# Kernel optimization log

Measured on AMD Instinct MI355X. Metric: run time of the kernel, lower is better.

The kernel has to match this reference:

```python
import jax, jax.numpy as jnp
import numpy as np

B_, S, D_IN, D_OUT, N_ADP, R = 4, 4096, 2048, 2048, 4, 16
SCALE = 32.0 / 16.0  # lora_alpha / r, use_rslora=False, same for all adaptors


def setup_inputs() -> dict:
    key = jax.random.key(0)
    ks = jax.random.split(key, 6)
    x = jax.random.normal(ks[0], (B_, S, D_IN), dtype=jnp.float32)
    mask = jax.random.uniform(ks[1], (N_ADP, B_, S, 1), dtype=jnp.float32)
    W = jax.random.normal(ks[2], (D_OUT, D_IN), dtype=jnp.float32) * 0.02
    b = jnp.zeros((D_OUT,), dtype=jnp.float32)
    A = jax.random.normal(ks[3], (N_ADP, R, D_IN), dtype=jnp.float32) * 0.02
    Bw = jax.random.normal(ks[4], (N_ADP, D_OUT, R), dtype=jnp.float32) * 0.02
    return {"x": x, "mask": mask, "W": W, "b": b, "A": A, "Bw": Bw}


def reference(x, mask, W, b, A, Bw):
    # base_layer: y = x @ W^T + b  -> [B, S, D_OUT]
    result = jnp.einsum('bsd,od->bso', x, W) + b
    # all adaptors batched: h = lora_A(x) -> [N, B, S, R]
    h = jnp.einsum('bsd,nrd->nbsr', x, A)
    # delta = lora_B(h) -> [N, B, S, D_OUT]
    delta = jnp.einsum('nbsr,nor->nbso', h, Bw)
    # scale, per-adaptor mask multiply, accumulate into residual
    result = result + jnp.sum(delta * SCALE * mask, axis=0)
    return result
```

## Files before the change

### kernel.cpp

```cpp
#include <hip/hip_runtime.h>
#include <stdint.h>


typedef __attribute__((ext_vector_type(8))) short bf16x8;
typedef __attribute__((ext_vector_type(4))) float f32x4;
typedef __attribute__((ext_vector_type(4))) unsigned short u16x4;
typedef __attribute__((ext_vector_type(8))) unsigned short u16x8;

#define GAS __attribute__((address_space(1)))
#define LAS __attribute__((address_space(3)))

static constexpr int BB   = 4;
static constexpr int SS   = 4096;
static constexpr int DIN  = 2048;
static constexpr int DOUT = 2048;
static constexpr int NADP = 4;
static constexpr int RR   = 16;
static constexpr int M    = BB * SS;
static constexpr int KA   = DIN + NADP * RR;
static constexpr float SCALE = 2.0f;

static constexpr int KSPLIT = 4;
static constexpr int KCH    = DIN / KSPLIT;

static constexpr int NT = KA / 64;
static constexpr int HT = 128 * 64;

static_assert(KA % 64 == 0, "K-loop needs BK=64 divisibility");
static_assert(NT >= 2, "pipeline needs >=2 K-steps");

__device__ __forceinline__ unsigned short f2bf(float f) {
  union { float f; uint32_t u; } v; v.f = f;
  uint32_t u = v.u;
  return (unsigned short)((u + 0x7FFFu + ((u >> 16) & 1u)) >> 16);
}

__global__ __launch_bounds__(256) void pass1a_conv_hpart(
    const float* __restrict__ x, const float* __restrict__ A,
    unsigned short* __restrict__ Xaug, float* __restrict__ Hpart)
{
  __shared__ unsigned short xb[64 * 64];
  __shared__ unsigned short ab[64 * 64];

  const int tid = threadIdx.x;
  const int rb = blockIdx.x >> 2;
  const int ks = blockIdx.x & 3;
  const int rowBase = rb * 64;
  const int kBase = ks * KCH;
  const int w = tid >> 6, lane = tid & 63;
  const int quad = lane >> 4, m16 = lane & 15;

  f32x4 acc[4];
  #pragma unroll
  for (int j = 0; j < 4; ++j) acc[j] = f32x4{0.f, 0.f, 0.f, 0.f};

  for (int kc = kBase; kc < kBase + KCH; kc += 64) {
    __syncthreads();
    #pragma unroll
    for (int l = 0; l < 4; ++l) {
      int v = l * 256 + tid;
      int r = v >> 4;
      int k = (v & 15) * 4;
      float4 xv = *(const float4*)(x + (size_t)(rowBase + r) * DIN + kc + k);
      u16x4 xq = { f2bf(xv.x), f2bf(xv.y), f2bf(xv.z), f2bf(xv.w) };
      *(u16x4*)(xb + r * 64 + k) = xq;
      *(u16x4*)(Xaug + (size_t)(rowBase + r) * KA + kc + k) = xq;
      float4 av = *(const float4*)(A + (size_t)r * DIN + kc + k);
      u16x4 aq = { f2bf(av.x), f2bf(av.y), f2bf(av.z), f2bf(av.w) };
      *(u16x4*)(ab + r * 64 + k) = aq;
    }
    __syncthreads();
    #pragma unroll
    for (int s = 0; s < 2; ++s) {
      bf16x8 af = *(const bf16x8*)(xb + (w * 16 + m16) * 64 + s * 32 + quad * 8);
      #pragma unroll
      for (int jt = 0; jt < 4; ++jt) {
        bf16x8 bfg = *(const bf16x8*)(ab + (jt * 16 + m16) * 64 + s * 32 + quad * 8);
        acc[jt] = __builtin_amdgcn_mfma_f32_16x16x32_bf16(af, bfg, acc[jt], 0, 0, 0);
      }
    }
  }

  const int grow0 = rowBase + w * 16 + quad * 4;
  #pragma unroll
  for (int jt = 0; jt < 4; ++jt) {
    #pragma unroll
    for (int r = 0; r < 4; ++r) {
      int grow = grow0 + r;
      Hpart[(((size_t)ks * M + grow) << 6) + jt * 16 + m16] = acc[jt][r];
    }
  }
}

__global__ __launch_bounds__(256) void pass1b_reduce_mask(
    const float* __restrict__ Hpart, const float* __restrict__ mask,
    unsigned short* __restrict__ Xaug)
{
  const int idx = blockIdx.x * 256 + threadIdx.x;
  const int row = idx >> 6;
  const int j   = idx & 63;
  float s = 0.f;
  #pragma unroll
  for (int ks = 0; ks < KSPLIT; ++ks)
    s += Hpart[(((size_t)ks * M) << 6) + idx];
  s *= mask[(size_t)(j >> 4) * M + row];
  Xaug[(size_t)row * KA + DIN + j] = f2bf(s);
}

__global__ __launch_bounds__(256) void pass2_wcvt(
    const float* __restrict__ W, const float* __restrict__ Bw,
    unsigned short* __restrict__ Waug)
{
  const int idx = blockIdx.x * 256 + threadIdx.x;
  const int row = idx >> 8;
  const int k   = (idx & 255) * 8;
  float4 a = *(const float4*)(W + (size_t)row * DIN + k);
  float4 b = *(const float4*)(W + (size_t)row * DIN + k + 4);
  u16x8 q = { f2bf(a.x), f2bf(a.y), f2bf(a.z), f2bf(a.w),
              f2bf(b.x), f2bf(b.y), f2bf(b.z), f2bf(b.w) };
  *(u16x8*)(Waug + (size_t)row * KA + k) = q;

  if (idx < DOUT * NADP) {
    const int col = idx >> 2, n = idx & 3;
    const float* src = Bw + (size_t)n * DOUT * RR + (size_t)col * RR;
    #pragma unroll
    for (int t = 0; t < 4; ++t) {
      float4 bv = *(const float4*)(src + 4 * t);
      u16x4 qq = { f2bf(SCALE * bv.x), f2bf(SCALE * bv.y),
                   f2bf(SCALE * bv.z), f2bf(SCALE * bv.w) };
      *(u16x4*)(Waug + (size_t)col * KA + DIN + n * 16 + 4 * t) = qq;
    }
  }
}

struct Stg { int so, dofs; };

__device__ __forceinline__ void gate_barrier() {
  __builtin_amdgcn_sched_barrier(0);
  __builtin_amdgcn_s_barrier();
  __builtin_amdgcn_sched_barrier(0);
}

__device__ __forceinline__ void stage_half(
    const unsigned short* __restrict__ g, unsigned short* l, int koff,
    const Stg& st)
{
  __builtin_amdgcn_global_load_lds((const GAS void*)(g + st.so + koff),
                                   (LAS void*)(l + st.dofs), 16, 0, 0);
  __builtin_amdgcn_global_load_lds((const GAS void*)(g + st.so + 64 * KA + koff),
                                   (LAS void*)(l + st.dofs + 4096), 16, 0, 0);
}

template<int VM1, int VM3, bool S>
__device__ __forceinline__ void kstep(int t,
    const unsigned short* __restrict__ ga, const unsigned short* __restrict__ gb,
    unsigned short* la, unsigned short* lb, const Stg& st,
    int rowA, int rowB, const int (&cc)[2], f32x4 (&acc)[8][4])
{
  const int cp = (t & 1) * (2 * HT);
  const int np = cp ^ (2 * HT);
  const unsigned short* A0 = la + cp;
  const unsigned short* A1 = la + cp + HT;
  const unsigned short* B0 = lb + cp;
  const unsigned short* B1 = lb + cp + HT;
  bf16x8 af[4][2], bA[2][2], bB[2][2];

  if (S) {
    stage_half(ga, la + np, (t + 1) * 64, st);
    stage_half(gb, lb + np, (t + 1) * 64, st);
    stage_half(gb + 128 * KA, lb + np + HT, (t + 1) * 64, st);
  }
  #pragma unroll
  for (int i = 0; i < 4; ++i)
    #pragma unroll
    for (int kk = 0; kk < 2; ++kk)
      af[i][kk] = *(const bf16x8*)(A0 + rowA + i * 1024 + cc[kk]);
  #pragma unroll
  for (int j = 0; j < 2; ++j)
    #pragma unroll
    for (int kk = 0; kk < 2; ++kk) {
      bA[j][kk] = *(const bf16x8*)(B0 + rowB + j * 1024 + cc[kk]);
      bB[j][kk] = *(const bf16x8*)(B1 + rowB + j * 1024 + cc[kk]);
    }
  __builtin_amdgcn_s_setprio(1);
  #pragma unroll
  for (int kk = 0; kk < 2; ++kk)
    #pragma unroll
    for (int i = 0; i < 4; ++i)
      #pragma unroll
      for (int j = 0; j < 2; ++j) {
        acc[i][j]     = __builtin_amdgcn_mfma_f32_16x16x32_bf16(af[i][kk], bA[j][kk], acc[i][j], 0, 0, 0);
        acc[i][2 + j] = __builtin_amdgcn_mfma_f32_16x16x32_bf16(af[i][kk], bB[j][kk], acc[i][2 + j], 0, 0, 0);
      }
  __builtin_amdgcn_s_setprio(0);
  asm volatile("s_waitcnt vmcnt(%0)" :: "i"(VM1) : "memory");
  gate_barrier();

  if (S) stage_half(ga + 128 * KA, la + np + HT, (t + 1) * 64, st);
  #pragma unroll
  for (int i = 0; i < 4; ++i)
    #pragma unroll
    for (int kk = 0; kk < 2; ++kk)
      af[i][kk] = *(const bf16x8*)(A1 + rowA + i * 1024 + cc[kk]);
  __builtin_amdgcn_s_setprio(1);
  #pragma unroll
  for (int kk = 0; kk < 2; ++kk)
    #pragma unroll
    for (int i = 0; i < 4; ++i)
      #pragma unroll
      for (int j = 0; j < 2; ++j) {
        acc[4 + i][j]     = __builtin_amdgcn_mfma_f32_16x16x32_bf16(af[i][kk], bA[j][kk], acc[4 + i][j], 0, 0, 0);
        acc[4 + i][2 + j] = __builtin_amdgcn_mfma_f32_16x16x32_bf16(af[i][kk], bB[j][kk], acc[4 + i][2 + j], 0, 0, 0);
      }
  __builtin_amdgcn_s_setprio(0);
  if constexpr (VM3 >= 0) {
    asm volatile("s_waitcnt vmcnt(%0)" :: "i"(VM3) : "memory");
    gate_barrier();
  }
}

__global__ __launch_bounds__(512, 2) void gemm_aug(
    const unsigned short* __restrict__ Xa, const unsigned short* __restrict__ Wa,
    const float* __restrict__ bias, float* __restrict__ out)
{
  __shared__ unsigned short lds_a[4 * HT];
  __shared__ unsigned short lds_b[4 * HT];

  const int tid = threadIdx.x;
  const int lin = ((int)blockIdx.x & 7) * 64 + ((int)blockIdx.x >> 3);
  const int bm = lin >> 3, bn = lin & 7;
  const int w = tid >> 6, lane = tid & 63;
  const int wm = w >> 2, wn = w & 3;
  const int quad = lane >> 4, m16 = lane & 15;

  f32x4 acc[8][4];
  #pragma unroll
  for (int i = 0; i < 8; ++i)
    #pragma unroll
    for (int j = 0; j < 4; ++j) acc[i][j] = f32x4{0.f, 0.f, 0.f, 0.f};

  const unsigned short* ga = Xa + (size_t)bm * 256 * KA;
  const unsigned short* gb = Wa + (size_t)bn * 256 * KA;

  Stg st;
  {
    int r = tid >> 3, c = (tid & 7) ^ (r & 7);
    st.so   = r * KA + c * 8;
    st.dofs = (tid & ~63) * 8;
  }

  int cc[2];
  cc[0] = (quad ^ (m16 & 7)) * 8;
  cc[1] = ((4 + quad) ^ (m16 & 7)) * 8;
  const int rowA = (wm * 64 + m16) * 64;
  const int rowB = (wn * 32 + m16) * 64;

  stage_half(ga, lds_a, 0, st);
  stage_half(gb, lds_b, 0, st);
  stage_half(gb + 128 * KA, lds_b + HT, 0, st);
  stage_half(ga + 128 * KA, lds_a + HT, 0, st);
  asm volatile("s_waitcnt vmcnt(2)" ::: "memory");
  gate_barrier();

  for (int t = 0; t < NT - 1; ++t)
    kstep<6, 2, true>(t, ga, gb, lds_a, lds_b, st, rowA, rowB, cc, acc);
  kstep<0, -1, false>(NT - 1, ga, gb, lds_a, lds_b, st, rowA, rowB, cc, acc);

  float bv[4];
  #pragma unroll
  for (int jj = 0; jj < 4; ++jj)
    bv[jj] = bias[bn * 256 + (jj >> 1) * 128 + wn * 32 + (jj & 1) * 16 + m16];
  #pragma unroll
  for (int I = 0; I < 8; ++I) {
    const int row0 = bm * 256 + (I >> 2) * 128 + wm * 64 + (I & 3) * 16 + quad * 4;
    #pragma unroll
    for (int jj = 0; jj < 4; ++jj) {
      const int col = bn * 256 + (jj >> 1) * 128 + wn * 32 + (jj & 1) * 16 + m16;
      #pragma unroll
      for (int r = 0; r < 4; ++r)
        out[(size_t)(row0 + r) * DOUT + col] = acc[I][jj][r] + bv[jj];
    }
  }
}

extern "C" void kernel_launch(void* const* d_in, const int* in_sizes, int n_in,
                              void* d_out, int out_size, void* d_ws, size_t ws_size,
                              hipStream_t stream) {
  const float* x    = (const float*)d_in[0];
  const float* mask = (const float*)d_in[1];
  const float* W    = (const float*)d_in[2];
  const float* bias = (const float*)d_in[3];
  const float* A    = (const float*)d_in[4];
  const float* Bw   = (const float*)d_in[5];
  float* out = (float*)d_out;

  unsigned short* Xaug = (unsigned short*)d_ws;
  unsigned short* Waug = Xaug + (size_t)M * KA;
  float* Hpart = (float*)(Waug + (size_t)DOUT * KA);

  pass1a_conv_hpart<<<dim3(M / 64 * KSPLIT), dim3(256), 0, stream>>>(x, A, Xaug, Hpart);
  pass1b_reduce_mask<<<dim3(M * 64 / 256), dim3(256), 0, stream>>>(Hpart, mask, Xaug);
  pass2_wcvt<<<dim3((DOUT * (DIN / 8)) / 256), dim3(256), 0, stream>>>(W, Bw, Waug);
  gemm_aug<<<dim3(512), dim3(512), 0, stream>>>(Xaug, Waug, bias, out);
}
```

Before: 428.3 us.

## Restructure GEMM K-loop into four-phase ping-pong schedule with deeper prefetch

Splits each K-step into four MFMA sub-phases (one per A-half/B-half quadrant), each bracketed by barriers and lgkmcnt waits. Global-to-LDS staging is spread across the phases, and two of the four half-tiles are prefetched two K-steps ahead into the slot the current step has just finished reading. This aims to overlap loads with MFMA work more evenly and to cut register pressure from B fragments. In exchange it adds more barriers per K-step and a more complicated tail that requires at least three K-tiles.

```diff
diff --git a/kernel.cpp b/kernel.cpp
--- a/kernel.cpp
+++ b/kernel.cpp
@@ -27,7 +27,7 @@
 static constexpr int HT = 128 * 64;
 
 static_assert(KA % 64 == 0, "K-loop needs BK=64 divisibility");
-static_assert(NT >= 2, "pipeline needs >=2 K-steps");
+static_assert(NT >= 3, "pipeline tail assumes >=3 K-tiles");
 
 __device__ __forceinline__ unsigned short f2bf(float f) {
   union { float f; uint32_t u; } v; v.f = f;
@@ -135,9 +135,13 @@
 
 struct Stg { int so, dofs; };
 
-__device__ __forceinline__ void gate_barrier() {
+__device__ __forceinline__ void bar() {
   __builtin_amdgcn_sched_barrier(0);
   __builtin_amdgcn_s_barrier();
+  __builtin_amdgcn_sched_barrier(0);
+}
+__device__ __forceinline__ void lgkm0() {
+  asm volatile("s_waitcnt lgkmcnt(0)" ::: "memory");
   __builtin_amdgcn_sched_barrier(0);
 }
 
@@ -151,7 +155,7 @@
                                    (LAS void*)(l + st.dofs + 4096), 16, 0, 0);
 }
 
-template<int VM1, int VM3, bool S>
+template<int VM, bool S01, bool S23>
 __device__ __forceinline__ void kstep(int t,
     const unsigned short* __restrict__ ga, const unsigned short* __restrict__ gb,
     unsigned short* la, unsigned short* lb, const Stg& st,
@@ -163,13 +167,8 @@
   const unsigned short* A1 = la + cp + HT;
   const unsigned short* B0 = lb + cp;
   const unsigned short* B1 = lb + cp + HT;
-  bf16x8 af[4][2], bA[2][2], bB[2][2];
-
-  if (S) {
-    stage_half(ga, la + np, (t + 1) * 64, st);
-    stage_half(gb, lb + np, (t + 1) * 64, st);
-    stage_half(gb + 128 * KA, lb + np + HT, (t + 1) * 64, st);
-  }
+  bf16x8 af[4][2], b[2][2];
+
   #pragma unroll
   for (int i = 0; i < 4; ++i)
     #pragma unroll
@@ -178,45 +177,76 @@
   #pragma unroll
   for (int j = 0; j < 2; ++j)
     #pragma unroll
-    for (int kk = 0; kk < 2; ++kk) {
-      bA[j][kk] = *(const bf16x8*)(B0 + rowB + j * 1024 + cc[kk]);
-      bB[j][kk] = *(const bf16x8*)(B1 + rowB + j * 1024 + cc[kk]);
-    }
+    for (int kk = 0; kk < 2; ++kk)
+      b[j][kk] = *(const bf16x8*)(B0 + rowB + j * 1024 + cc[kk]);
+  if (S01) stage_half(gb, lb + np, (t + 1) * 64, st);
+  bar(); lgkm0();
   __builtin_amdgcn_s_setprio(1);
   #pragma unroll
   for (int kk = 0; kk < 2; ++kk)
     #pragma unroll
     for (int i = 0; i < 4; ++i)
       #pragma unroll
-      for (int j = 0; j < 2; ++j) {
-        acc[i][j]     = __builtin_amdgcn_mfma_f32_16x16x32_bf16(af[i][kk], bA[j][kk], acc[i][j], 0, 0, 0);
-        acc[i][2 + j] = __builtin_amdgcn_mfma_f32_16x16x32_bf16(af[i][kk], bB[j][kk], acc[i][2 + j], 0, 0, 0);
-      }
+      for (int j = 0; j < 2; ++j)
+        acc[i][j] = __builtin_amdgcn_mfma_f32_16x16x32_bf16(af[i][kk], b[j][kk], acc[i][j], 0, 0, 0);
   __builtin_amdgcn_s_setprio(0);
-  asm volatile("s_waitcnt vmcnt(%0)" :: "i"(VM1) : "memory");
-  gate_barrier();
-
-  if (S) stage_half(ga + 128 * KA, la + np + HT, (t + 1) * 64, st);
+  bar();
+
+  #pragma unroll
+  for (int j = 0; j < 2; ++j)
+    #pragma unroll
+    for (int kk = 0; kk < 2; ++kk)
+      b[j][kk] = *(const bf16x8*)(B1 + rowB + j * 1024 + cc[kk]);
+  if (S01) stage_half(ga + 128 * KA, la + np + HT, (t + 1) * 64, st);
+  bar(); lgkm0();
+  __builtin_amdgcn_s_setprio(1);
+  #pragma unroll
+  for (int kk = 0; kk < 2; ++kk)
+    #pragma unroll
+    for (int i = 0; i < 4; ++i)
+      #pragma unroll
+      for (int j = 0; j < 2; ++j)
+        acc[i][2 + j] = __builtin_amdgcn_mfma_f32_16x16x32_bf16(af[i][kk], b[j][kk], acc[i][2 + j], 0, 0, 0);
+  __builtin_amdgcn_s_setprio(0);
+  bar();
+
   #pragma unroll
   for (int i = 0; i < 4; ++i)
     #pragma unroll
     for (int kk = 0; kk < 2; ++kk)
       af[i][kk] = *(const bf16x8*)(A1 + rowA + i * 1024 + cc[kk]);
+  if (S23) stage_half(ga, la + cp, (t + 2) * 64, st);
+  bar(); lgkm0();
   __builtin_amdgcn_s_setprio(1);
   #pragma unroll
   for (int kk = 0; kk < 2; ++kk)
     #pragma unroll
     for (int i = 0; i < 4; ++i)
       #pragma unroll
-      for (int j = 0; j < 2; ++j) {
-        acc[4 + i][j]     = __builtin_amdgcn_mfma_f32_16x16x32_bf16(af[i][kk], bA[j][kk], acc[4 + i][j], 0, 0, 0);
-        acc[4 + i][2 + j] = __builtin_amdgcn_mfma_f32_16x16x32_bf16(af[i][kk], bB[j][kk], acc[4 + i][2 + j], 0, 0, 0);
-      }
+      for (int j = 0; j < 2; ++j)
+        acc[4 + i][2 + j] = __builtin_amdgcn_mfma_f32_16x16x32_bf16(af[i][kk], b[j][kk], acc[4 + i][2 + j], 0, 0, 0);
   __builtin_amdgcn_s_setprio(0);
-  if constexpr (VM3 >= 0) {
-    asm volatile("s_waitcnt vmcnt(%0)" :: "i"(VM3) : "memory");
-    gate_barrier();
-  }
+  bar();
+
+  #pragma unroll
+  for (int j = 0; j < 2; ++j)
+    #pragma unroll
+    for (int kk = 0; kk < 2; ++kk)
+      b[j][kk] = *(const bf16x8*)(B0 + rowB + j * 1024 + cc[kk]);
+  if (S23) stage_half(gb + 128 * KA, lb + cp + HT, (t + 2) * 64, st);
+  bar(); lgkm0();
+  __builtin_amdgcn_s_setprio(1);
+  #pragma unroll
+  for (int kk = 0; kk < 2; ++kk)
+    #pragma unroll
+    for (int i = 0; i < 4; ++i)
+      #pragma unroll
+      for (int j = 0; j < 2; ++j)
+        acc[4 + i][j] = __builtin_amdgcn_mfma_f32_16x16x32_bf16(af[i][kk], b[j][kk], acc[4 + i][j], 0, 0, 0);
+  __builtin_amdgcn_s_setprio(0);
+  if constexpr (VM >= 0)
+    asm volatile("s_waitcnt vmcnt(%0)" :: "i"(VM) : "memory");
+  bar();
 }
 
 __global__ __launch_bounds__(512, 2) void gemm_aug(
@@ -259,12 +289,15 @@
   stage_half(gb, lds_b, 0, st);
   stage_half(gb + 128 * KA, lds_b + HT, 0, st);
   stage_half(ga + 128 * KA, lds_a + HT, 0, st);
-  asm volatile("s_waitcnt vmcnt(2)" ::: "memory");
-  gate_barrier();
-
-  for (int t = 0; t < NT - 1; ++t)
-    kstep<6, 2, true>(t, ga, gb, lds_a, lds_b, st, rowA, rowB, cc, acc);
-  kstep<0, -1, false>(NT - 1, ga, gb, lds_a, lds_b, st, rowA, rowB, cc, acc);
+  stage_half(ga, lds_a + 2 * HT, 64, st);
+  stage_half(gb + 128 * KA, lds_b + 3 * HT, 64, st);
+  asm volatile("s_waitcnt vmcnt(4)" ::: "memory");
+  bar();
+
+  for (int t = 0; t < NT - 2; ++t)
+    kstep<4, true, true>(t, ga, gb, lds_a, lds_b, st, rowA, rowB, cc, acc);
+  kstep<0, true, false>(NT - 2, ga, gb, lds_a, lds_b, st, rowA, rowB, cc, acc);
+  kstep<-1, false, false>(NT - 1, ga, gb, lds_a, lds_b, st, rowA, rowB, cc, acc);
 
   float bv[4];
   #pragma unroll
```

Measured after the change: 431.9 us. No clear change (+0.8%).
